# Performance work log

Measured on AMD Instinct MI355X. Metric: run time of the kernel, lower is better.

## Reference

```python
import jax, jax.numpy as jnp
import numpy as np

NUM_HEADS = 16
NUM_KV_HEADS = 4
HEAD_SIZE = 128
SCALE = 1.0 / np.sqrt(128.0).astype(np.float32)
NEG_INF = -1e30


def setup_inputs() -> dict:
    key = jax.random.key(0)
    kq, kk, kv = jax.random.split(key, 3)
    B, S = 2, 2048
    query = jax.random.normal(kq, (B, NUM_HEADS, S, HEAD_SIZE), dtype=jnp.float32)
    k = jax.random.normal(kk, (B, NUM_KV_HEADS, S, HEAD_SIZE), dtype=jnp.float32)
    v = jax.random.normal(kv, (B, NUM_KV_HEADS, S, HEAD_SIZE), dtype=jnp.float32)
    return {"query": query, "key": k, "value": v}


def _attn(query, key, value):
    # query: [B, H, S, D]; key/value: [B, Hkv, S, D]; GQA with group = H // Hkv
    B, H, S, D = query.shape
    Hkv = key.shape[1]
    G = H // Hkv
    q = query.reshape(B, Hkv, G, S, D)
    # scores: [B, Hkv, G, Sq, Sk]
    scores = jnp.einsum('bkgsd,bktd->bkgst', q, key) * jnp.float32(SCALE)
    causal = jnp.tril(jnp.ones((S, S), dtype=bool))  # [Sq, Sk]
    scores = jnp.where(causal, scores, jnp.float32(NEG_INF))
    probs = jax.nn.softmax(scores, axis=-1)
    out = jnp.einsum('bkgst,bktd->bkgsd', probs, value)  # [B, Hkv, G, S, D]
    out = out.reshape(B, H, S, D)
    # transpose(1,2).reshape -> [B, S, H*D]
    return out.transpose(0, 2, 1, 3).reshape(B, S, H * D)


def reference(query, key, value):
    return _attn(query, key, value)
```

## Files before the change

### kernel.cpp

```cpp
#include <hip/hip_runtime.h>


#define S_LEN 2048
#define DH    128
#define NH    16
#define NKVH  4
#define NB    2
#define TQ    128
#define TK    64
#define NQT   (S_LEN / TQ)
#define QSCALE 0.12752749610559243f

typedef __attribute__((ext_vector_type(8))) short short8;
typedef __attribute__((ext_vector_type(4))) float f32x4;

#if __has_builtin(__builtin_amdgcn_exp2f)
#define EX2(x) __builtin_amdgcn_exp2f(x)
#else
#define EX2(x) exp2f(x)
#endif

__device__ __forceinline__ unsigned pk2(float a, float b) {
    union { float f; unsigned u; } x, y; x.f = a; y.f = b;
    return ((x.u + 0x8000u) >> 16) | ((y.u + 0x8000u) & 0xffff0000u);
}
__device__ __forceinline__ void cp16(const void* g, void* lds) {
    __builtin_amdgcn_global_load_lds(
        (const __attribute__((address_space(1))) void*)g,
        (__attribute__((address_space(3))) void*)lds, 16, 0, 0);
}

__global__ __launch_bounds__(256, 4)
void prepack(const float* __restrict__ K, const float* __restrict__ V,
             unsigned short* __restrict__ Kb, unsigned short* __restrict__ Vt) {
    if (blockIdx.y == 0) {
        const long long flat = (long long)blockIdx.x * 2048 + threadIdx.x * 8;
        const int s = (int)(flat >> 7) & (S_LEN - 1);
        const int d0 = (int)flat & 127;
        const float* p = K + flat;
        float4 x = *(const float4*)p;
        float4 y = *(const float4*)(p + 4);
        const int cs = (d0 >> 3) ^ (s & 7);
        uint4 o;
        o.x = pk2(x.x, x.y); o.y = pk2(x.z, x.w);
        o.z = pk2(y.x, y.y); o.w = pk2(y.z, y.w);
        *(uint4*)(Kb + (flat & ~127LL) + cs * 8) = o;
    } else {
        const int x = blockIdx.x;
        const int bkvh = x >> 7, sblk = (x >> 2) & 31, q = x & 3;
        const int tid = threadIdx.x;
        __shared__ unsigned Lt[64][17];
        const float* base = V + (size_t)bkvh * S_LEN * DH + (size_t)sblk * 64 * DH + q * 32;
#pragma unroll
        for (int j = 0; j < 2; ++j) {
            const int e = tid + j * 256;
            const int s = e >> 3, c4 = e & 7;
            float4 v = *(const float4*)(base + (size_t)s * DH + c4 * 4);
            Lt[s][c4 * 2]     = pk2(v.x, v.y);
            Lt[s][c4 * 2 + 1] = pk2(v.z, v.w);
        }
        __syncthreads();
        const unsigned short* lt = (const unsigned short*)&Lt[0][0];
        const int d_loc = tid >> 3, pc = tid & 7;
        const int d = q * 32 + d_loc;
        const int c_log = pc ^ (d & 7);
        unsigned short vv[8];
#pragma unroll
        for (int j = 0; j < 8; ++j) {
            const int kp = c_log * 8 + j;
            const int kv = (kp & 3) * 16 + (kp >> 2);
            vv[j] = lt[kv * 34 + d_loc];
        }
        uint4 o;
        o.x = (unsigned)vv[0] | ((unsigned)vv[1] << 16);
        o.y = (unsigned)vv[2] | ((unsigned)vv[3] << 16);
        o.z = (unsigned)vv[4] | ((unsigned)vv[5] << 16);
        o.w = (unsigned)vv[6] | ((unsigned)vv[7] << 16);
        *(uint4*)(Vt + (size_t)bkvh * S_LEN * DH + (size_t)d * S_LEN + sblk * 64 + pc * 8) = o;
    }
}

__global__ __launch_bounds__(512, 4)
void attn_fwd(const float* __restrict__ Q,
              const unsigned short* __restrict__ Kb,
              const unsigned short* __restrict__ Vtg,
              float* __restrict__ O,
              float* __restrict__ Opart,
              float* __restrict__ Lpart) {
    const int n    = blockIdx.x;
    const int g    = n & 7;
    const int b    = g >> 2;
    const int kvh  = g & 3;
    const int kk   = n >> 3;
    const int h    = kvh * 4 + (kk & 3);
    const int pr   = kk >> 2;
    const int a    = pr & 7;
    const int role = pr >> 3;
    const int sid  = ((b * NH + h) << 3) + a;

    const int tid  = threadIdx.x;
    const int w    = tid >> 6;
    const int lane = tid & 63;
    const int quad = lane >> 4;
    const int l16  = lane & 15;
    const int swz  = l16 & 7;

    int qt0, kt00, nr0, qt1; bool two_seg;
    if (role == 0) { qt0 = a;      kt00 = 0;         nr0 = 2 * a + 2;
                     qt1 = 15 - a; two_seg = true; }
    else           { qt0 = 15 - a; kt00 = 15 - 2*a;  nr0 = 17;
                     qt1 = 0;      two_seg = false; }

    __shared__ alignas(16) unsigned short Kl[2][TK][DH];
    __shared__ alignas(16) unsigned short Vl[2][DH][TK];
    __shared__ alignas(16) unsigned short Pl[TQ][64];

    const unsigned short* kb = Kb  + ((size_t)b * NKVH + kvh) * (size_t)(S_LEN * DH);
    const unsigned short* vb = Vtg + ((size_t)b * NKVH + kvh) * (size_t)(S_LEN * DH);

    auto stage = [&](int buf, int kt) {
        const char* ks = (const char*)(kb + (size_t)kt * TK * DH);
        char* kd = (char*)&Kl[buf][0][0];
#pragma unroll
        for (int i = 0; i < 2; ++i) {
            const int off = w * 2048 + i * 1024;
            cp16(ks + off + lane * 16, kd + off);
        }
        const char* vs = (const char*)vb + (size_t)kt * (TK * 2);
        char* vd = (char*)&Vl[buf][0][0];
#pragma unroll
        for (int i = 0; i < 2; ++i) {
            const int off = w * 2048 + i * 1024;
            const int row = w * 16 + i * 8 + (lane >> 3);
            cp16(vs + (size_t)row * (S_LEN * 2) + (lane & 7) * 16, vd + off);
        }
    };
    auto ktof = [&](int r) { return r < nr0 ? kt00 + r : r - nr0; };

    stage(0, ktof(0));

    int qt  = qt0;
    int wq0 = qt * TQ + w * 16;
    int ntw = 2 * qt + 1 + (w >> 2);

    short8 aq[4];
    auto loadQ = [&]() {
        const float* qp = Q + (((size_t)b * NH + h) * S_LEN + wq0 + l16) * DH;
#pragma unroll
        for (int dc = 0; dc < 4; ++dc) {
            float4 xx = *(const float4*)(qp + dc * 32 + quad * 8);
            float4 yy = *(const float4*)(qp + dc * 32 + quad * 8 + 4);
            union { unsigned u[4]; short8 s; } tq;
            tq.u[0] = pk2(xx.x * QSCALE, xx.y * QSCALE);
            tq.u[1] = pk2(xx.z * QSCALE, xx.w * QSCALE);
            tq.u[2] = pk2(yy.x * QSCALE, yy.y * QSCALE);
            tq.u[3] = pk2(yy.z * QSCALE, yy.w * QSCALE);
            aq[dc] = tq.s;
        }
    };
    loadQ();

    f32x4 o[8];
    float lsum[4];
#pragma unroll
    for (int ch = 0; ch < 8; ++ch) o[ch] = (f32x4){0.f, 0.f, 0.f, 0.f};
#pragma unroll
    for (int r = 0; r < 4; ++r) lsum[r] = 0.f;

    __syncthreads();

    int cur = 0;
    for (int r = 0; r < 17; ++r) {
        if (r + 1 < 17) stage(cur ^ 1, ktof(r + 1));
        const int kt = ktof(r);
        if (kt < ntw) {
            const int j0 = kt * TK;
            const bool diag = (kt == ntw - 1);
            f32x4 s[4];
#pragma unroll
            for (int k4 = 0; k4 < 4; ++k4) s[k4] = (f32x4){0.f, 0.f, 0.f, 0.f};
#pragma unroll
            for (int dc = 0; dc < 4; ++dc) {
#pragma unroll
                for (int k4 = 0; k4 < 4; ++k4) {
                    short8 bk = *(const short8*)&Kl[cur][k4 * 16 + l16][((dc * 4 + quad) ^ swz) * 8];
                    s[k4] = __builtin_amdgcn_mfma_f32_16x16x32_bf16(aq[dc], bk, s[k4], 0, 0, 0);
                }
            }
            {
                const int rb = wq0 + quad * 4;
#pragma unroll
                for (int rr = 0; rr < 4; ++rr) {
                    float v0 = s[0][rr], v1 = s[1][rr];
                    float v2 = s[2][rr], v3 = s[3][rr];
                    if (diag) {
                        const int row = rb + rr;
                        if (j0 + l16      > row) v0 = -1e30f;
                        if (j0 + 16 + l16 > row) v1 = -1e30f;
                        if (j0 + 32 + l16 > row) v2 = -1e30f;
                        if (j0 + 48 + l16 > row) v3 = -1e30f;
                    }
                    float p0 = EX2(v0), p1 = EX2(v1), p2 = EX2(v2), p3 = EX2(v3);
                    lsum[rr] += (p0 + p1) + (p2 + p3);
                    const int prow = w * 16 + quad * 4 + rr;
                    const int wcol = (l16 * 8) ^ ((prow & 7) << 4);
                    *(uint2*)((char*)&Pl[0][0] + prow * 128 + wcol) =
                        make_uint2(pk2(p0, p1), pk2(p2, p3));
                }
            }
            const int rx = (l16 & 7) << 4;
#pragma unroll
            for (int kc = 0; kc < 2; ++kc) {
                const int cb = kc * 64 + quad * 16;
                short8 ap = *(const short8*)((const char*)&Pl[0][0] + (w * 16 + l16) * 128 + (cb ^ rx));
#pragma unroll
                for (int ch = 0; ch < 8; ++ch) {
                    short8 bv = *(const short8*)&Vl[cur][ch * 16 + l16][((kc * 4 + quad) ^ swz) * 8];
                    o[ch] = __builtin_amdgcn_mfma_f32_16x16x32_bf16(ap, bv, o[ch], 0, 0, 0);
                }
            }
        }
        __syncthreads();
        cur ^= 1;
        if (two_seg && r == nr0 - 1) {
#pragma unroll
            for (int rr = 0; rr < 4; ++rr) {
                float rs = lsum[rr];
                rs += __shfl_xor(rs, 1);
                rs += __shfl_xor(rs, 2);
                rs += __shfl_xor(rs, 4);
                rs += __shfl_xor(rs, 8);
                const float invl = 1.f / rs;
                const int row = wq0 + quad * 4 + rr;
                float* op = O + ((size_t)b * S_LEN + row) * (NH * DH) + h * DH;
#pragma unroll
                for (int ch = 0; ch < 8; ++ch)
                    op[ch * 16 + l16] = o[ch][rr] * invl;
            }
            qt = qt1; wq0 = qt * TQ + w * 16; ntw = 2 * qt + 1 + (w >> 2);
            loadQ();
#pragma unroll
            for (int ch = 0; ch < 8; ++ch) o[ch] = (f32x4){0.f, 0.f, 0.f, 0.f};
#pragma unroll
            for (int rr = 0; rr < 4; ++rr) lsum[rr] = 0.f;
        }
    }

    float* lb = Lpart + (size_t)(role * 256 + sid) * 128;
#pragma unroll
    for (int rr = 0; rr < 4; ++rr) {
        float rs = lsum[rr];
        rs += __shfl_xor(rs, 1);
        rs += __shfl_xor(rs, 2);
        rs += __shfl_xor(rs, 4);
        rs += __shfl_xor(rs, 8);
        const int rl = w * 16 + quad * 4 + rr;
        if (l16 == 0) lb[rl] = rs;
        float* op;
        if (role == 0) {
            const int row = wq0 + quad * 4 + rr;
            op = O + ((size_t)b * S_LEN + row) * (NH * DH) + h * DH;
        } else {
            op = Opart + (size_t)sid * (128 * 128) + (size_t)rl * 128;
        }
#pragma unroll
        for (int ch = 0; ch < 8; ++ch)
            op[ch * 16 + l16] = o[ch][rr];
    }
}

__global__ __launch_bounds__(256)
void combine(const float* __restrict__ Opart, const float* __restrict__ Lpart,
             float* __restrict__ O) {
    const int blk = blockIdx.x;
    const int sid = blk >> 2;
    const int qp  = blk & 3;
    const int bh = sid >> 3, a = sid & 7;
    const int b = bh >> 4, h = bh & 15;
    const int qt = 15 - a;
    const float* o1 = Opart + (size_t)sid * (128 * 128);
    const float* l0 = Lpart + (size_t)sid * 128;
    const float* l1 = Lpart + (size_t)(256 + sid) * 128;
    const int tid = threadIdx.x;
#pragma unroll
    for (int i = 0; i < 4; ++i) {
        const int idx = qp * 1024 + i * 256 + tid;
        const int row = idx >> 5;
        const int c4  = idx & 31;
        const float inv = 1.f / (l0[row] + l1[row]);
        float* op = O + ((size_t)b * S_LEN + qt * 128 + row) * (NH * DH) + h * DH + c4 * 4;
        const float4 x = *(const float4*)op;
        const float4 y = ((const float4*)o1)[idx];
        float4 z;
        z.x = (x.x + y.x) * inv; z.y = (x.y + y.y) * inv;
        z.z = (x.z + y.z) * inv; z.w = (x.w + y.w) * inv;
        *(float4*)op = z;
    }
}

extern "C" void kernel_launch(void* const* d_in, const int* in_sizes, int n_in,
                              void* d_out, int out_size, void* d_ws, size_t ws_size,
                              hipStream_t stream) {
    const float* Q = (const float*)d_in[0];
    const float* K = (const float*)d_in[1];
    const float* V = (const float*)d_in[2];
    float* O = (float*)d_out;
    unsigned short* Kb = (unsigned short*)d_ws;
    unsigned short* Vt = Kb + (size_t)NB * NKVH * S_LEN * DH;
    float* Opart = (float*)(Vt + (size_t)NB * NKVH * S_LEN * DH);
    float* Lpart = Opart + (size_t)256 * 128 * 128;
    dim3 pgrid(NB * NKVH * (S_LEN / 16), 2);
    prepack<<<pgrid, 256, 0, stream>>>(K, V, Kb, Vt);
    attn_fwd<<<dim3(512), 512, 0, stream>>>(Q, Kb, Vt, O, Opart, Lpart);
    combine<<<dim3(1024), 256, 0, stream>>>(Opart, Lpart, O);
}
```

Measured before the change: 148.1 us.

## Keep softmax probabilities in registers by computing transposed QK^T scores

Swaps the MFMA operands for the QK^T product so each lane holds scores laid out to feed the PV MFMA as its A operand directly. This removes the shared-memory P buffer with its writes and reads, and lets the row sum be reduced with fewer shuffles. The V transpose permutation is changed to match the new key ordering inside each fragment. It saves LDS traffic and space but depends on the permuted V layout being exactly right.

Result: no change. 146.6 us (-1.0%).

```diff
diff --git a/kernel.cpp b/kernel.cpp
--- a/kernel.cpp
+++ b/kernel.cpp
@@ -68,7 +68,8 @@
 #pragma unroll
         for (int j = 0; j < 8; ++j) {
             const int kp = c_log * 8 + j;
-            const int kv = (kp & 3) * 16 + (kp >> 2);
+            const int kv = ((kp >> 5) & 1) * 32 + ((kp >> 2) & 1) * 16
+                         + ((kp >> 3) & 3) * 4 + (kp & 3);
             vv[j] = lt[kv * 34 + d_loc];
         }
         uint4 o;
@@ -113,7 +114,6 @@
 
     __shared__ alignas(16) unsigned short Kl[2][TK][DH];
     __shared__ alignas(16) unsigned short Vl[2][DH][TK];
-    __shared__ alignas(16) unsigned short Pl[TQ][64];
 
     const unsigned short* kb = Kb  + ((size_t)b * NKVH + kvh) * (size_t)(S_LEN * DH);
     const unsigned short* vb = Vtg + ((size_t)b * NKVH + kvh) * (size_t)(S_LEN * DH);
@@ -161,11 +161,9 @@
     loadQ();
 
     f32x4 o[8];
-    float lsum[4];
+    float lsum = 0.f;
 #pragma unroll
     for (int ch = 0; ch < 8; ++ch) o[ch] = (f32x4){0.f, 0.f, 0.f, 0.f};
-#pragma unroll
-    for (int r = 0; r < 4; ++r) lsum[r] = 0.f;
 
     __syncthreads();
 
@@ -184,53 +182,44 @@
 #pragma unroll
                 for (int k4 = 0; k4 < 4; ++k4) {
                     short8 bk = *(const short8*)&Kl[cur][k4 * 16 + l16][((dc * 4 + quad) ^ swz) * 8];
-                    s[k4] = __builtin_amdgcn_mfma_f32_16x16x32_bf16(aq[dc], bk, s[k4], 0, 0, 0);
+                    s[k4] = __builtin_amdgcn_mfma_f32_16x16x32_bf16(bk, aq[dc], s[k4], 0, 0, 0);
                 }
             }
-            {
-                const int rb = wq0 + quad * 4;
+            const int qrow = wq0 + l16;
+            float p[4][4];
+#pragma unroll
+            for (int k4 = 0; k4 < 4; ++k4) {
 #pragma unroll
                 for (int rr = 0; rr < 4; ++rr) {
-                    float v0 = s[0][rr], v1 = s[1][rr];
-                    float v2 = s[2][rr], v3 = s[3][rr];
-                    if (diag) {
-                        const int row = rb + rr;
-                        if (j0 + l16      > row) v0 = -1e30f;
-                        if (j0 + 16 + l16 > row) v1 = -1e30f;
-                        if (j0 + 32 + l16 > row) v2 = -1e30f;
-                        if (j0 + 48 + l16 > row) v3 = -1e30f;
-                    }
-                    float p0 = EX2(v0), p1 = EX2(v1), p2 = EX2(v2), p3 = EX2(v3);
-                    lsum[rr] += (p0 + p1) + (p2 + p3);
-                    const int prow = w * 16 + quad * 4 + rr;
-                    const int wcol = (l16 * 8) ^ ((prow & 7) << 4);
-                    *(uint2*)((char*)&Pl[0][0] + prow * 128 + wcol) =
-                        make_uint2(pk2(p0, p1), pk2(p2, p3));
+                    float v = s[k4][rr];
+                    if (diag && (j0 + k4 * 16 + quad * 4 + rr > qrow)) v = -1e30f;
+                    const float pe = EX2(v);
+                    lsum += pe;
+                    p[k4][rr] = pe;
                 }
             }
-            const int rx = (l16 & 7) << 4;
-#pragma unroll
-            for (int kc = 0; kc < 2; ++kc) {
-                const int cb = kc * 64 + quad * 16;
-                short8 ap = *(const short8*)((const char*)&Pl[0][0] + (w * 16 + l16) * 128 + (cb ^ rx));
-#pragma unroll
-                for (int ch = 0; ch < 8; ++ch) {
-                    short8 bv = *(const short8*)&Vl[cur][ch * 16 + l16][((kc * 4 + quad) ^ swz) * 8];
-                    o[ch] = __builtin_amdgcn_mfma_f32_16x16x32_bf16(ap, bv, o[ch], 0, 0, 0);
-                }
+            union { unsigned u[4]; short8 s8; } pa0, pa1;
+            pa0.u[0] = pk2(p[0][0], p[0][1]); pa0.u[1] = pk2(p[0][2], p[0][3]);
+            pa0.u[2] = pk2(p[1][0], p[1][1]); pa0.u[3] = pk2(p[1][2], p[1][3]);
+            pa1.u[0] = pk2(p[2][0], p[2][1]); pa1.u[1] = pk2(p[2][2], p[2][3]);
+            pa1.u[2] = pk2(p[3][0], p[3][1]); pa1.u[3] = pk2(p[3][2], p[3][3]);
+#pragma unroll
+            for (int ch = 0; ch < 8; ++ch) {
+                short8 bv0 = *(const short8*)&Vl[cur][ch * 16 + l16][(quad ^ swz) * 8];
+                o[ch] = __builtin_amdgcn_mfma_f32_16x16x32_bf16(pa0.s8, bv0, o[ch], 0, 0, 0);
+                short8 bv1 = *(const short8*)&Vl[cur][ch * 16 + l16][((4 + quad) ^ swz) * 8];
+                o[ch] = __builtin_amdgcn_mfma_f32_16x16x32_bf16(pa1.s8, bv1, o[ch], 0, 0, 0);
             }
         }
         __syncthreads();
         cur ^= 1;
         if (two_seg && r == nr0 - 1) {
+            float rs = lsum;
+            rs += __shfl_xor(rs, 16);
+            rs += __shfl_xor(rs, 32);
 #pragma unroll
             for (int rr = 0; rr < 4; ++rr) {
-                float rs = lsum[rr];
-                rs += __shfl_xor(rs, 1);
-                rs += __shfl_xor(rs, 2);
-                rs += __shfl_xor(rs, 4);
-                rs += __shfl_xor(rs, 8);
-                const float invl = 1.f / rs;
+                const float invl = 1.f / __shfl(rs, quad * 4 + rr);
                 const int row = wq0 + quad * 4 + rr;
                 float* op = O + ((size_t)b * S_LEN + row) * (NH * DH) + h * DH;
 #pragma unroll
@@ -241,31 +230,30 @@
             loadQ();
 #pragma unroll
             for (int ch = 0; ch < 8; ++ch) o[ch] = (f32x4){0.f, 0.f, 0.f, 0.f};
-#pragma unroll
-            for (int rr = 0; rr < 4; ++rr) lsum[rr] = 0.f;
+            lsum = 0.f;
         }
     }
 
     float* lb = Lpart + (size_t)(role * 256 + sid) * 128;
-#pragma unroll
-    for (int rr = 0; rr < 4; ++rr) {
-        float rs = lsum[rr];
-        rs += __shfl_xor(rs, 1);
-        rs += __shfl_xor(rs, 2);
-        rs += __shfl_xor(rs, 4);
-        rs += __shfl_xor(rs, 8);
-        const int rl = w * 16 + quad * 4 + rr;
-        if (l16 == 0) lb[rl] = rs;
-        float* op;
-        if (role == 0) {
-            const int row = wq0 + quad * 4 + rr;
-            op = O + ((size_t)b * S_LEN + row) * (NH * DH) + h * DH;
-        } else {
-            op = Opart + (size_t)sid * (128 * 128) + (size_t)rl * 128;
-        }
-#pragma unroll
-        for (int ch = 0; ch < 8; ++ch)
-            op[ch * 16 + l16] = o[ch][rr];
+    {
+        float rs = lsum;
+        rs += __shfl_xor(rs, 16);
+        rs += __shfl_xor(rs, 32);
+        if (lane < 16) lb[w * 16 + l16] = rs;
+#pragma unroll
+        for (int rr = 0; rr < 4; ++rr) {
+            const int rl = w * 16 + quad * 4 + rr;
+            float* op;
+            if (role == 0) {
+                const int row = wq0 + quad * 4 + rr;
+                op = O + ((size_t)b * S_LEN + row) * (NH * DH) + h * DH;
+            } else {
+                op = Opart + (size_t)sid * (128 * 128) + (size_t)rl * 128;
+            }
+#pragma unroll
+            for (int ch = 0; ch < 8; ++ch)
+                op[ch * 16 + l16] = o[ch][rr];
+        }
     }
 }
 
```
